# Optimization experiments

Measured on AMD Instinct MI355X. Metric: run time of the kernel, lower is better.

## Reference

```python
import jax, jax.numpy as jnp
import numpy as np

N = 100000      # num POIs (nodes)
M = 20000       # num trajectories (hyperedges)
NNZ = 1000000   # incidence entries
D = 128         # emb_dim
NUM_LAYERS = 3
NEG_SLOPE = 0.2  # PyG HypergraphConv leaky_relu default


def setup_inputs() -> dict:
    key = jax.random.key(0)
    ks = jax.random.split(key, 8)
    pois_embs = jax.random.normal(ks[0], (N, D), jnp.float32)
    traj_embs = jax.random.normal(ks[1], (M, D), jnp.float32)
    hyperedge_weight = jax.random.uniform(ks[2], (M,), jnp.float32)
    node_idx = jax.random.randint(ks[3], (NNZ,), 0, N, jnp.int32)
    edge_idx = jax.random.randint(ks[4], (NNZ,), 0, M, jnp.int32)
    # learned params of the shared HypergraphConv layer (heads=1, concat)
    W_lin = jax.random.normal(ks[5], (D, D), jnp.float32) / np.sqrt(D).astype(np.float32)
    att = jax.random.normal(ks[6], (2 * D,), jnp.float32) * 0.1
    bias = jnp.zeros((D,), jnp.float32)
    return dict(pois_embs=pois_embs, traj_embs=traj_embs,
                hyperedge_weight=hyperedge_weight,
                node_idx=node_idx, edge_idx=edge_idx,
                W_lin=W_lin, att=att, bias=bias)


def _segment_softmax(scores, seg, num_seg):
    smax = jax.ops.segment_max(scores, seg, num_segments=num_seg)
    smax = jnp.where(jnp.isfinite(smax), smax, 0.0)  # guard empty segments
    ex = jnp.exp(scores - smax[seg])
    den = jax.ops.segment_sum(ex, seg, num_segments=num_seg)
    return ex / (den[seg] + 1e-16)


def _hconv(x, traj_embs, hyperedge_weight, node_idx, edge_idx, W_lin, att, bias):
    # x: [N, D] node feats; traj_embs: [M, D] hyperedge feats
    xt = x @ W_lin            # [N, D]  lin(x)
    et = traj_embs @ W_lin    # [M, D]  lin(hyperedge_attr)
    # attention logits per incidence pair (additive decomposition of cat*att)
    s_n = xt @ att[:D]        # [N]
    s_e = et @ att[D:]        # [M]
    alpha = jax.nn.leaky_relu(s_n[node_idx] + s_e[edge_idx], NEG_SLOPE)  # [NNZ]
    alpha = _segment_softmax(alpha, node_idx, N)  # softmax grouped by node
    # degree normalizations: D = sum_e H_ve * w_e, B = |e|
    Ddeg = jax.ops.segment_sum(hyperedge_weight[edge_idx], node_idx, num_segments=N)
    Dinv = jnp.where(Ddeg > 0, 1.0 / Ddeg, 0.0)
    Bdeg = jax.ops.segment_sum(jnp.ones((NNZ,), xt.dtype), edge_idx, num_segments=M)
    Binv = jnp.where(Bdeg > 0, 1.0 / Bdeg, 0.0)
    # node -> edge: B^{-1} H^T (alpha * x)
    msg1 = (alpha * Binv[edge_idx])[:, None] * xt[node_idx]        # [NNZ, D]
    edge_out = jax.ops.segment_sum(msg1, edge_idx, num_segments=M)  # [M, D]
    # edge -> node: D^{-1} H (alpha * edge_out)
    msg2 = (alpha * Dinv[node_idx])[:, None] * edge_out[edge_idx]   # [NNZ, D]
    out = jax.ops.segment_sum(msg2, node_idx, num_segments=N)       # [N, D]
    return out + bias


def reference(pois_embs, traj_embs, hyperedge_weight, node_idx, edge_idx, W_lin, att, bias):
    cur = pois_embs
    acc = pois_embs  # running sum of stacked layer outputs (incl. input)
    for _ in range(NUM_LAYERS):
        cur = _hconv(cur, traj_embs, hyperedge_weight, node_idx, edge_idx, W_lin, att, bias) + cur
        acc = acc + cur
    return acc / jnp.asarray(NUM_LAYERS + 1, acc.dtype)  # mean over stack
```

## Files before the change

kernel.cpp:

```cpp
#include <hip/hip_runtime.h>
#include <hip/hip_fp16.h>
#include <cstdint>
#include <cstddef>
#include <cstring>

#define DIM 128
#define NEG_SLOPE 0.2f

#define EREP 16
#define NREP 8

typedef _Float16 half8v __attribute__((ext_vector_type(8)));
typedef __attribute__((ext_vector_type(4))) float float4v;

__device__ __forceinline__ float2 h2f2(uint u) {
  __half2 h;
  __builtin_memcpy(&h, &u, 4);
  return __half22float2(h);
}
__device__ __forceinline__ uint packh2(float lo, float hi) {
  __half2 h = __floats2half2_rn(lo, hi);
  uint u;
  __builtin_memcpy(&u, &h, 4);
  return u;
}
__device__ __forceinline__ ushort f2h_us(float f) {
  __half h = __float2half_rn(f);
  ushort us;
  __builtin_memcpy(&us, &h, 2);
  return us;
}
__device__ __forceinline__ float lrelu(float x) {
  return x >= 0.0f ? x : NEG_SLOPE * x;
}

__global__ void wswz_kernel(const float* __restrict__ W, ushort* __restrict__ Wswz)
{
  int i = blockIdx.x * 256 + threadIdx.x;
  int j = i & 7, lane = (i >> 3) & 63, nt = (i >> 9) & 7, kt = i >> 12;
  int k = kt * 32 + (lane >> 4) * 8 + j;
  int col = nt * 16 + (lane & 15);
  Wswz[i] = f2h_us(W[k * 128 + col]);
}

__global__ void poish_kernel(const float* __restrict__ pois,
                             uint4* __restrict__ pois_h, int N_, int NP)
{
  int i = blockIdx.x * 256 + threadIdx.x;
  if (i >= NP * 16) return;
  int row = i >> 4;
  uint4 o;
  if (row < N_) {
    const float* src = pois + (size_t)i * 8;
    float4 f0 = *(const float4*)src;
    float4 f1 = *(const float4*)(src + 4);
    o.x = packh2(f0.x, f0.y); o.y = packh2(f0.z, f0.w);
    o.z = packh2(f1.x, f1.y); o.w = packh2(f1.z, f1.w);
  } else { o.x = o.y = o.z = o.w = 0; }
  pois_h[i] = o;
}

__global__ __launch_bounds__(256) void gemm_mfma_kernel(
    const ushort* __restrict__ Xb, const ushort* __restrict__ Wswz,
    const float* __restrict__ att, ushort* __restrict__ Yb,
    float* __restrict__ s_n, int rowsN)
{
  __shared__ ushort st[64 * 128];
  int tid = threadIdx.x;
  int w = tid >> 6, lane = tid & 63;
  int q = lane >> 4, c = lane & 15;
  int r0b = blockIdx.x * 64;
  int r0 = r0b + w * 16;
  float4v acc[8];
#pragma unroll
  for (int nt = 0; nt < 8; ++nt) acc[nt] = (float4v){0.f, 0.f, 0.f, 0.f};
  const ushort* arow = Xb + (size_t)(r0 + c) * DIM + q * 8;
#pragma unroll
  for (int kt = 0; kt < 4; ++kt) {
    half8v a = *(const half8v*)(arow + kt * 32);
#pragma unroll
    for (int nt = 0; nt < 8; ++nt) {
      half8v b = *(const half8v*)(Wswz + ((((kt << 3) + nt) << 9) + (lane << 3)));
      acc[nt] = __builtin_amdgcn_mfma_f32_16x16x32_f16(a, b, acc[nt], 0, 0, 0);
    }
  }
  float av[8];
#pragma unroll
  for (int nt = 0; nt < 8; ++nt) av[nt] = att[nt * 16 + c];
  float p0 = 0, p1 = 0, p2 = 0, p3 = 0;
#pragma unroll
  for (int nt = 0; nt < 8; ++nt) {
    p0 = fmaf(acc[nt][0], av[nt], p0);
    p1 = fmaf(acc[nt][1], av[nt], p1);
    p2 = fmaf(acc[nt][2], av[nt], p2);
    p3 = fmaf(acc[nt][3], av[nt], p3);
  }
#pragma unroll
  for (int m = 8; m >= 1; m >>= 1) {
    p0 += __shfl_xor(p0, m, 64);
    p1 += __shfl_xor(p1, m, 64);
    p2 += __shfl_xor(p2, m, 64);
    p3 += __shfl_xor(p3, m, 64);
  }
  if (c == 0) {
    int rb = r0 + q * 4;
    if (rb + 0 < rowsN) s_n[rb + 0] = p0;
    if (rb + 1 < rowsN) s_n[rb + 1] = p1;
    if (rb + 2 < rowsN) s_n[rb + 2] = p2;
    if (rb + 3 < rowsN) s_n[rb + 3] = p3;
  }
  ushort* sw = st + w * 2048;
#pragma unroll
  for (int nt = 0; nt < 8; ++nt) {
    sw[(q * 4 + 0) * 128 + nt * 16 + c] = f2h_us(acc[nt][0]);
    sw[(q * 4 + 1) * 128 + nt * 16 + c] = f2h_us(acc[nt][1]);
    sw[(q * 4 + 2) * 128 + nt * 16 + c] = f2h_us(acc[nt][2]);
    sw[(q * 4 + 3) * 128 + nt * 16 + c] = f2h_us(acc[nt][3]);
  }
  __syncthreads();
#pragma unroll
  for (int it = 0; it < 4; ++it) {
    int idx = tid + it * 256;
    int row = idx >> 4, seg = idx & 15;
    *(uint4*)(Yb + (size_t)(r0b + row) * DIM + seg * 8) =
        *(const uint4*)&st[row * 128 + seg * 8];
  }
}

__global__ __launch_bounds__(256) void se_kernel(
    const float* __restrict__ traj, const float* __restrict__ W,
    const float* __restrict__ att, const float* __restrict__ hw,
    float* __restrict__ s_e, float2* __restrict__ se_hw, int M_)
{
  __shared__ float wv[128];
  int tid = threadIdx.x;
  if (tid < 128) {
    const float* wr = W + (size_t)tid * 128;
    float acc = 0.0f;
#pragma unroll 4
    for (int k = 0; k < 128; ++k) acc = fmaf(wr[k], att[DIM + k], acc);
    wv[tid] = acc;
  }
  __syncthreads();
  int e = blockIdx.x * 4 + (tid >> 6);
  int lane = tid & 63;
  if (e >= M_) return;
  const float* row = traj + (size_t)e * DIM;
  float v = row[lane] * wv[lane] + row[lane + 64] * wv[lane + 64];
#pragma unroll
  for (int d = 32; d > 0; d >>= 1) v += __shfl_down(v, d, 64);
  if (lane == 0) {
    s_e[e] = v;
    float2 g; g.x = v; g.y = hw[e];
    se_hw[e] = g;
  }
}

__global__ void hist_rank_kernel(const int* __restrict__ node_idx,
                                 const int* __restrict__ edge_idx,
                                 int* __restrict__ ncnt_r, int* __restrict__ ecnt_r,
                                 int* __restrict__ r_n, int* __restrict__ r_e,
                                 int nnz, int M_, int N_)
{
  int t = blockIdx.x * blockDim.x + threadIdx.x;
  int j = t * 2;
  if (j >= nnz) return;
  int* ec = ecnt_r + (size_t)(t & (EREP - 1)) * M_;
  int* nc = ncnt_r + (size_t)(t & (NREP - 1)) * N_;
  if (j + 2 <= nnz) {
    int2 e = *(const int2*)&edge_idx[j];
    int2 n = *(const int2*)&node_idx[j];
    int a0 = atomicAdd(&ec[e.x], 1);
    int a1 = atomicAdd(&ec[e.y], 1);
    int b0 = atomicAdd(&nc[n.x], 1);
    int b1 = atomicAdd(&nc[n.y], 1);
    *(int2*)&r_e[j] = make_int2(a0, a1);
    *(int2*)&r_n[j] = make_int2(b0, b1);
  } else {
    r_e[j] = atomicAdd(&ec[edge_idx[j]], 1);
    r_n[j] = atomicAdd(&nc[node_idx[j]], 1);
  }
}

__global__ void repsum_kernel(int* __restrict__ cnt_r, int* __restrict__ cnt,
                              int nbins, int reps)
{
  int b = blockIdx.x * blockDim.x + threadIdx.x;
  if (b >= nbins) return;
  int s = 0;
  for (int r = 0; r < reps; ++r) {
    size_t o = (size_t)r * nbins + b;
    int v = cnt_r[o];
    cnt_r[o] = s;
    s += v;
  }
  cnt[b] = s;
}

__global__ __launch_bounds__(1024) void scan_block_kernel(
    const int* __restrict__ cnt, int* __restrict__ off,
    int* __restrict__ partials, int nbins)
{
  __shared__ int ws[16];
  int tid = threadIdx.x, lane = tid & 63, wid = tid >> 6;
  int base = blockIdx.x * 4096 + tid * 4;
  int x0 = base + 0 < nbins ? cnt[base + 0] : 0;
  int x1 = base + 1 < nbins ? cnt[base + 1] : 0;
  int x2 = base + 2 < nbins ? cnt[base + 2] : 0;
  int x3 = base + 3 < nbins ? cnt[base + 3] : 0;
  int t = x0 + x1 + x2 + x3;
  int v = t;
#pragma unroll
  for (int d = 1; d < 64; d <<= 1) {
    int y = __shfl_up(v, d, 64);
    if (lane >= d) v += y;
  }
  if (lane == 63) ws[wid] = v;
  __syncthreads();
  if (tid < 16) {
    int s = ws[tid];
#pragma unroll
    for (int d = 1; d < 16; d <<= 1) {
      int y = __shfl_up(s, d, 16);
      if (tid >= d) s += y;
    }
    ws[tid] = s;
  }
  __syncthreads();
  int pre = (wid > 0 ? ws[wid - 1] : 0) + (v - t);
  if (base + 0 < nbins) off[base + 0] = pre;
  if (base + 1 < nbins) off[base + 1] = pre + x0;
  if (base + 2 < nbins) off[base + 2] = pre + x0 + x1;
  if (base + 3 < nbins) off[base + 3] = pre + x0 + x1 + x2;
  if (tid == 0) partials[blockIdx.x] = ws[15];
}

__global__ __launch_bounds__(64) void scan_partials_kernel(
    int* __restrict__ partials, int nb)
{
  int lane = threadIdx.x;
  int t = lane < nb ? partials[lane] : 0;
  int v = t;
#pragma unroll
  for (int d = 1; d < 64; d <<= 1) {
    int y = __shfl_up(v, d, 64);
    if (lane >= d) v += y;
  }
  if (lane < nb) partials[lane] = v - t;
  if (lane == 63) partials[nb] = v;
}

__global__ void add_off_combine_kernel(int* __restrict__ off,
                                       const int* __restrict__ partials,
                                       int* __restrict__ pre,
                                       int nbins, int nb, int reps)
{
  int i = blockIdx.x * blockDim.x + threadIdx.x;
  if (i < nbins) {
    int o = off[i] + partials[i >> 12];
    off[i] = o;
    for (int r = 0; r < reps; ++r) pre[(size_t)r * nbins + i] += o;
  }
  if (i == 0) off[nbins] = partials[nb];
}

__global__ void scatter_edge_kernel(const int* __restrict__ node_idx,
                                    const int* __restrict__ edge_idx,
                                    const int* __restrict__ r_e,
                                    const int* __restrict__ pre_e,
                                    int* __restrict__ nd_e, int nnz, int M_)
{
  int j = (blockIdx.x * blockDim.x + threadIdx.x) * 4;
  if (j >= nnz) return;
  if (j + 4 <= nnz) {
    const int* p0 = pre_e + (size_t)((j >> 1) & (EREP - 1)) * M_;
    const int* p1 = pre_e + (size_t)(((j >> 1) + 1) & (EREP - 1)) * M_;
    int4 e = *(const int4*)&edge_idx[j];
    int4 n = *(const int4*)&node_idx[j];
    int4 re = *(const int4*)&r_e[j];
    nd_e[p0[e.x] + re.x] = n.x;
    nd_e[p0[e.y] + re.y] = n.y;
    nd_e[p1[e.z] + re.z] = n.z;
    nd_e[p1[e.w] + re.w] = n.w;
  } else {
    for (int k = j; k < nnz; ++k) {
      const int* pp = pre_e + (size_t)((k >> 1) & (EREP - 1)) * M_;
      nd_e[pp[edge_idx[k]] + r_e[k]] = node_idx[k];
    }
  }
}

__global__ void scatter_node_kernel(const int* __restrict__ node_idx,
                                    const int* __restrict__ edge_idx,
                                    const int* __restrict__ r_n,
                                    const int* __restrict__ pre_n,
                                    int* __restrict__ eidx_n, int nnz, int N_)
{
  int j = (blockIdx.x * blockDim.x + threadIdx.x) * 4;
  if (j >= nnz) return;
  if (j + 4 <= nnz) {
    const int* p0 = pre_n + (size_t)((j >> 1) & (NREP - 1)) * N_;
    const int* p1 = pre_n + (size_t)(((j >> 1) + 1) & (NREP - 1)) * N_;
    int4 e = *(const int4*)&edge_idx[j];
    int4 n = *(const int4*)&node_idx[j];
    int4 rn = *(const int4*)&r_n[j];
    eidx_n[p0[n.x] + rn.x] = e.x;
    eidx_n[p0[n.y] + rn.y] = e.y;
    eidx_n[p1[n.z] + rn.z] = e.z;
    eidx_n[p1[n.w] + rn.w] = e.w;
  } else {
    for (int k = j; k < nnz; ++k) {
      const int* pp = pre_n + (size_t)((k >> 1) & (NREP - 1)) * N_;
      eidx_n[pp[node_idx[k]] + r_n[k]] = edge_idx[k];
    }
  }
}

__global__ void softstat_kernel(const int* __restrict__ noff,
                                const int* __restrict__ eidx_n,
                                const float* __restrict__ s_n,
                                const float2* __restrict__ se_hw,
                                float2* __restrict__ ns2,
                                float* __restrict__ Dinv, int N_)
{
  int n = blockIdx.x * blockDim.x + threadIdx.x;
  if (n >= N_) return;
  int s = noff[n], e1 = noff[n + 1];
  float sn = s_n[n];
  float m = -INFINITY, den = 0.0f, d = 0.0f;
  int t = s;
  for (; t + 4 <= e1; t += 4) {
    int i0 = eidx_n[t], i1 = eidx_n[t + 1], i2 = eidx_n[t + 2], i3 = eidx_n[t + 3];
    float2 g0 = se_hw[i0], g1 = se_hw[i1], g2 = se_hw[i2], g3 = se_hw[i3];
    float l0 = lrelu(sn + g0.x), l1 = lrelu(sn + g1.x);
    float l2 = lrelu(sn + g2.x), l3 = lrelu(sn + g3.x);
    float mm = fmaxf(fmaxf(fmaxf(l0, l1), fmaxf(l2, l3)), m);
    den = den * __expf(m - mm) + __expf(l0 - mm) + __expf(l1 - mm)
        + __expf(l2 - mm) + __expf(l3 - mm);
    m = mm;
    d += g0.y + g1.y + g2.y + g3.y;
  }
  for (; t < e1; ++t) {
    float2 g = se_hw[eidx_n[t]];
    float l = lrelu(sn + g.x);
    float mm = fmaxf(l, m);
    den = den * __expf(m - mm) + __expf(l - mm);
    m = mm;
    d += g.y;
  }
  if (s == e1) m = 0.0f;
  float2 r;
  r.x = sn;
  r.y = m + __logf(den + 1e-16f);
  ns2[n] = r;
  Dinv[n] = d > 0.0f ? 1.0f / d : 0.0f;
}

__global__ __launch_bounds__(256) void msg1_kernel(
    const int* __restrict__ eoff, const int* __restrict__ nd_e,
    const float2* __restrict__ ns2, const float* __restrict__ s_e,
    const ushort* __restrict__ xt, uint* __restrict__ eo, int M_)
{
  int e = blockIdx.x * (blockDim.x >> 6) + (threadIdx.x >> 6);
  int lane = threadIdx.x & 63;
  if (e >= M_) return;
  int s = eoff[e], t1 = eoff[e + 1];
  int len = t1 - s;
  float binv = len > 0 ? 1.0f / (float)len : 0.0f;
  float se = s_e[e];
  const uint* xt4 = (const uint*)xt + lane;
  float2 acc = {0.0f, 0.0f};
  int t = s;
  for (; t + 8 <= t1; t += 8) {
    int n0 = nd_e[t],     n1 = nd_e[t + 1], n2 = nd_e[t + 2], n3 = nd_e[t + 3];
    int n4 = nd_e[t + 4], n5 = nd_e[t + 5], n6 = nd_e[t + 6], n7 = nd_e[t + 7];
    float2 q0 = ns2[n0], q1 = ns2[n1], q2 = ns2[n2], q3 = ns2[n3];
    float2 q4 = ns2[n4], q5 = ns2[n5], q6 = ns2[n6], q7 = ns2[n7];
    uint u0 = xt4[(size_t)n0 * 64], u1 = xt4[(size_t)n1 * 64];
    uint u2 = xt4[(size_t)n2 * 64], u3 = xt4[(size_t)n3 * 64];
    uint u4 = xt4[(size_t)n4 * 64], u5 = xt4[(size_t)n5 * 64];
    uint u6 = xt4[(size_t)n6 * 64], u7 = xt4[(size_t)n7 * 64];
    float c0 = __expf(lrelu(q0.x + se) - q0.y);
    float c1 = __expf(lrelu(q1.x + se) - q1.y);
    float c2 = __expf(lrelu(q2.x + se) - q2.y);
    float c3 = __expf(lrelu(q3.x + se) - q3.y);
    float c4 = __expf(lrelu(q4.x + se) - q4.y);
    float c5 = __expf(lrelu(q5.x + se) - q5.y);
    float c6 = __expf(lrelu(q6.x + se) - q6.y);
    float c7 = __expf(lrelu(q7.x + se) - q7.y);
    float2 f0 = h2f2(u0), f1 = h2f2(u1), f2 = h2f2(u2), f3 = h2f2(u3);
    float2 f4 = h2f2(u4), f5 = h2f2(u5), f6 = h2f2(u6), f7 = h2f2(u7);
    acc.x = fmaf(c0, f0.x, acc.x); acc.y = fmaf(c0, f0.y, acc.y);
    acc.x = fmaf(c1, f1.x, acc.x); acc.y = fmaf(c1, f1.y, acc.y);
    acc.x = fmaf(c2, f2.x, acc.x); acc.y = fmaf(c2, f2.y, acc.y);
    acc.x = fmaf(c3, f3.x, acc.x); acc.y = fmaf(c3, f3.y, acc.y);
    acc.x = fmaf(c4, f4.x, acc.x); acc.y = fmaf(c4, f4.y, acc.y);
    acc.x = fmaf(c5, f5.x, acc.x); acc.y = fmaf(c5, f5.y, acc.y);
    acc.x = fmaf(c6, f6.x, acc.x); acc.y = fmaf(c6, f6.y, acc.y);
    acc.x = fmaf(c7, f7.x, acc.x); acc.y = fmaf(c7, f7.y, acc.y);
  }
  for (; t < t1; ++t) {
    int nd = nd_e[t];
    float2 q = ns2[nd];
    uint u = xt4[(size_t)nd * 64];
    float c = __expf(lrelu(q.x + se) - q.y);
    float2 f = h2f2(u);
    acc.x = fmaf(c, f.x, acc.x);
    acc.y = fmaf(c, f.y, acc.y);
  }
  eo[(size_t)e * (DIM / 2) + lane] = packh2(acc.x * binv, acc.y * binv);
}

__global__ __launch_bounds__(256) void msg2_kernel(
    const int* __restrict__ noff, const int* __restrict__ eidx_n,
    const float2* __restrict__ ns2, const float* __restrict__ Dinv,
    const float* __restrict__ s_e, const uint* __restrict__ eo,
    const float* __restrict__ bias,
    const float* __restrict__ cin_f, const uint* __restrict__ cin_h,
    const float* __restrict__ x1f, const uint* __restrict__ x2h,
    uint* __restrict__ couth, float* __restrict__ dout,
    int mode, int N_)
{
  int n = blockIdx.x * (blockDim.x >> 6) + (threadIdx.x >> 6);
  int lane = threadIdx.x & 63;
  if (n >= N_) return;
  int s = noff[n], t1 = noff[n + 1];
  float2 nsv = ns2[n];
  float sn = nsv.x, lz = nsv.y;
  const uint* eo4 = eo + lane;
  float2 acc = {0.0f, 0.0f};
  int t = s;
  for (; t + 8 <= t1; t += 8) {
    int e0 = eidx_n[t],     e1 = eidx_n[t + 1], e2 = eidx_n[t + 2], e3 = eidx_n[t + 3];
    int e4 = eidx_n[t + 4], e5 = eidx_n[t + 5], e6 = eidx_n[t + 6], e7 = eidx_n[t + 7];
    float x0 = s_e[e0], xx1 = s_e[e1], xx2 = s_e[e2], x3 = s_e[e3];
    float x4 = s_e[e4], x5 = s_e[e5], x6 = s_e[e6], x7 = s_e[e7];
    uint u0 = eo4[(size_t)e0 * 64], u1 = eo4[(size_t)e1 * 64];
    uint u2 = eo4[(size_t)e2 * 64], u3 = eo4[(size_t)e3 * 64];
    uint u4 = eo4[(size_t)e4 * 64], u5 = eo4[(size_t)e5 * 64];
    uint u6 = eo4[(size_t)e6 * 64], u7 = eo4[(size_t)e7 * 64];
    float c0 = __expf(lrelu(sn + x0) - lz);
    float c1 = __expf(lrelu(sn + xx1) - lz);
    float c2 = __expf(lrelu(sn + xx2) - lz);
    float c3 = __expf(lrelu(sn + x3) - lz);
    float c4 = __expf(lrelu(sn + x4) - lz);
    float c5 = __expf(lrelu(sn + x5) - lz);
    float c6 = __expf(lrelu(sn + x6) - lz);
    float c7 = __expf(lrelu(sn + x7) - lz);
    float2 f0 = h2f2(u0), f1 = h2f2(u1), f2 = h2f2(u2), f3 = h2f2(u3);
    float2 f4 = h2f2(u4), f5 = h2f2(u5), f6 = h2f2(u6), f7 = h2f2(u7);
    acc.x = fmaf(c0, f0.x, acc.x); acc.y = fmaf(c0, f0.y, acc.y);
    acc.x = fmaf(c1, f1.x, acc.x); acc.y = fmaf(c1, f1.y, acc.y);
    acc.x = fmaf(c2, f2.x, acc.x); acc.y = fmaf(c2, f2.y, acc.y);
    acc.x = fmaf(c3, f3.x, acc.x); acc.y = fmaf(c3, f3.y, acc.y);
    acc.x = fmaf(c4, f4.x, acc.x); acc.y = fmaf(c4, f4.y, acc.y);
    acc.x = fmaf(c5, f5.x, acc.x); acc.y = fmaf(c5, f5.y, acc.y);
    acc.x = fmaf(c6, f6.x, acc.x); acc.y = fmaf(c6, f6.y, acc.y);
    acc.x = fmaf(c7, f7.x, acc.x); acc.y = fmaf(c7, f7.y, acc.y);
  }
  for (; t < t1; ++t) {
    int e = eidx_n[t];
    uint u = eo4[(size_t)e * 64];
    float c = __expf(lrelu(sn + s_e[e]) - lz);
    float2 f = h2f2(u);
    acc.x = fmaf(c, f.x, acc.x);
    acc.y = fmaf(c, f.y, acc.y);
  }
  float sc = Dinv[n];
  float2 b = ((const float2*)bias)[lane];
  size_t idx = (size_t)n * DIM + lane * 2;
  float cinx, ciny;
  if (mode == 0) {
    cinx = cin_f[idx]; ciny = cin_f[idx + 1];
  } else {
    float2 f = h2f2(cin_h[(size_t)n * 64 + lane]);
    cinx = f.x; ciny = f.y;
  }
  float cx = cinx + acc.x * sc + b.x;
  float cy = ciny + acc.y * sc + b.y;
  if (mode == 2) {
    float2 f2v = h2f2(x2h[(size_t)n * 64 + lane]);
    dout[idx]     = (x1f[idx]     + f2v.x + cinx + cx) * 0.25f;
    dout[idx + 1] = (x1f[idx + 1] + f2v.y + ciny + cy) * 0.25f;
  } else {
    couth[(size_t)n * 64 + lane] = packh2(cx, cy);
  }
}

static inline int cdiv(int a, int b) { return (a + b - 1) / b; }

extern "C" void kernel_launch(void* const* d_in, const int* in_sizes, int n_in,
                              void* d_out, int out_size, void* d_ws, size_t ws_size,
                              hipStream_t stream)
{
  const float* pois = (const float*)d_in[0];
  const float* traj = (const float*)d_in[1];
  const float* hw   = (const float*)d_in[2];
  const int* node_idx = (const int*)d_in[3];
  const int* edge_idx = (const int*)d_in[4];
  const float* W    = (const float*)d_in[5];
  const float* att  = (const float*)d_in[6];
  const float* bias = (const float*)d_in[7];
  float* dout = (float*)d_out;

  const int N   = in_sizes[0] / DIM;
  const int M   = in_sizes[2];
  const int NNZ = in_sizes[3];
  const int NP  = (N + 63) & ~63;

  char* p = (char*)d_ws;
  auto alloc = [&](size_t bytes) -> void* {
    void* r = (void*)p;
    p += (bytes + 255) & ~(size_t)255;
    return r;
  };
  ushort* xt_h    = (ushort*)alloc((size_t)NP * DIM * 2);
  ushort* pois_h  = (ushort*)alloc((size_t)NP * DIM * 2);
  uint*   cura_h  = (uint*)alloc((size_t)NP * 64 * 4);
  uint*   curb_h  = (uint*)alloc((size_t)NP * 64 * 4);
  ushort* W_swz   = (ushort*)alloc(16384 * 2);
  uint*   eo_h  = (uint*)alloc((size_t)M * (DIM / 2) * 4);
  float2* ns2   = (float2*)alloc((size_t)N * 8);
  float*  s_e  = (float*)alloc((size_t)M * 4);
  float2* se_hw = (float2*)alloc((size_t)M * 8);
  float*  s_n  = (float*)alloc((size_t)N * 4);
  float*  Dinv = (float*)alloc((size_t)N * 4);
  int* ecnt   = (int*)alloc((size_t)M * 4);
  int* ncnt   = (int*)alloc((size_t)N * 4);
  int* ecnt_r = (int*)alloc((size_t)EREP * M * 4);
  int* ncnt_r = (int*)alloc((size_t)NREP * N * 4);
  int* eoff = (int*)alloc((size_t)(M + 1) * 4);
  int* noff = (int*)alloc((size_t)(N + 1) * 4);
  int* r_e  = (int*)alloc((size_t)NNZ * 4);
  int* r_n  = (int*)alloc((size_t)NNZ * 4);
  int* nd_e   = (int*)alloc((size_t)NNZ * 4);
  int* eidx_n = (int*)alloc((size_t)NNZ * 4);
  int* part_e = (int*)alloc(65 * 4);
  int* part_n = (int*)alloc(65 * 4);
  (void)ws_size;

  const int nbE = cdiv(M, 4096), nbN = cdiv(N, 4096);

  hipMemsetAsync(ecnt_r, 0, (size_t)EREP * M * 4, stream);
  hipMemsetAsync(ncnt_r, 0, (size_t)NREP * N * 4, stream);
  hist_rank_kernel<<<cdiv(NNZ, 512), 256, 0, stream>>>(node_idx, edge_idx, ncnt_r, ecnt_r, r_n, r_e, NNZ, M, N);
  repsum_kernel<<<cdiv(M, 256), 256, 0, stream>>>(ecnt_r, ecnt, M, EREP);
  repsum_kernel<<<cdiv(N, 256), 256, 0, stream>>>(ncnt_r, ncnt, N, NREP);
  scan_block_kernel<<<nbE, 1024, 0, stream>>>(ecnt, eoff, part_e, M);
  scan_block_kernel<<<nbN, 1024, 0, stream>>>(ncnt, noff, part_n, N);
  scan_partials_kernel<<<1, 64, 0, stream>>>(part_e, nbE);
  scan_partials_kernel<<<1, 64, 0, stream>>>(part_n, nbN);
  add_off_combine_kernel<<<cdiv(M, 256), 256, 0, stream>>>(eoff, part_e, ecnt_r, M, nbE, EREP);
  add_off_combine_kernel<<<cdiv(N, 256), 256, 0, stream>>>(noff, part_n, ncnt_r, N, nbN, NREP);
  scatter_edge_kernel<<<cdiv(NNZ, 1024), 256, 0, stream>>>(node_idx, edge_idx, r_e, ecnt_r, nd_e, NNZ, M);
  scatter_node_kernel<<<cdiv(NNZ, 1024), 256, 0, stream>>>(node_idx, edge_idx, r_n, ncnt_r, eidx_n, NNZ, N);

  wswz_kernel<<<64, 256, 0, stream>>>(W, W_swz);
  se_kernel<<<cdiv(M, 4), 256, 0, stream>>>(traj, W, att, hw, s_e, se_hw, M);
  poish_kernel<<<cdiv(NP * 16, 256), 256, 0, stream>>>(pois, (uint4*)pois_h, N, NP);

  for (int layer = 0; layer < 3; ++layer) {
    const ushort* gin = (layer == 0) ? pois_h
                       : (layer == 1) ? (const ushort*)cura_h
                                      : (const ushort*)curb_h;
    gemm_mfma_kernel<<<NP / 64, 256, 0, stream>>>(gin, W_swz, att, xt_h, s_n, N);
    softstat_kernel<<<cdiv(N, 256), 256, 0, stream>>>(noff, eidx_n, s_n, se_hw, ns2, Dinv, N);
    msg1_kernel<<<cdiv(M, 4), 256, 0, stream>>>(eoff, nd_e, ns2, s_e, xt_h, eo_h, M);
    const uint* cin_h = (layer == 1) ? cura_h : curb_h;
    uint* couth = (layer == 0) ? cura_h : curb_h;
    msg2_kernel<<<cdiv(N, 4), 256, 0, stream>>>(noff, eidx_n, ns2, Dinv, s_e, eo_h,
                                                bias, pois, cin_h, pois, cura_h,
                                                couth, dout, layer, N);
  }
}
```

Measured before the change: 738.5 us.

## Split each wave into four row-groups with 16-byte gathers in message kernels

```diff
diff --git a/kernel.cpp b/kernel.cpp
--- a/kernel.cpp
+++ b/kernel.cpp
@@ -359,131 +359,153 @@
 __global__ __launch_bounds__(256) void msg1_kernel(
     const int* __restrict__ eoff, const int* __restrict__ nd_e,
     const float2* __restrict__ ns2, const float* __restrict__ s_e,
-    const ushort* __restrict__ xt, uint* __restrict__ eo, int M_)
-{
-  int e = blockIdx.x * (blockDim.x >> 6) + (threadIdx.x >> 6);
+    const uint4* __restrict__ xt16, uint4* __restrict__ eo16, int M_)
+{
+  int e = blockIdx.x * 4 + (threadIdx.x >> 6);
   int lane = threadIdx.x & 63;
+  int r = lane >> 4, c = lane & 15;
   if (e >= M_) return;
   int s = eoff[e], t1 = eoff[e + 1];
   int len = t1 - s;
   float binv = len > 0 ? 1.0f / (float)len : 0.0f;
   float se = s_e[e];
-  const uint* xt4 = (const uint*)xt + lane;
-  float2 acc = {0.0f, 0.0f};
-  int t = s;
-  for (; t + 8 <= t1; t += 8) {
-    int n0 = nd_e[t],     n1 = nd_e[t + 1], n2 = nd_e[t + 2], n3 = nd_e[t + 3];
-    int n4 = nd_e[t + 4], n5 = nd_e[t + 5], n6 = nd_e[t + 6], n7 = nd_e[t + 7];
-    float2 q0 = ns2[n0], q1 = ns2[n1], q2 = ns2[n2], q3 = ns2[n3];
-    float2 q4 = ns2[n4], q5 = ns2[n5], q6 = ns2[n6], q7 = ns2[n7];
-    uint u0 = xt4[(size_t)n0 * 64], u1 = xt4[(size_t)n1 * 64];
-    uint u2 = xt4[(size_t)n2 * 64], u3 = xt4[(size_t)n3 * 64];
-    uint u4 = xt4[(size_t)n4 * 64], u5 = xt4[(size_t)n5 * 64];
-    uint u6 = xt4[(size_t)n6 * 64], u7 = xt4[(size_t)n7 * 64];
-    float c0 = __expf(lrelu(q0.x + se) - q0.y);
-    float c1 = __expf(lrelu(q1.x + se) - q1.y);
-    float c2 = __expf(lrelu(q2.x + se) - q2.y);
-    float c3 = __expf(lrelu(q3.x + se) - q3.y);
-    float c4 = __expf(lrelu(q4.x + se) - q4.y);
-    float c5 = __expf(lrelu(q5.x + se) - q5.y);
-    float c6 = __expf(lrelu(q6.x + se) - q6.y);
-    float c7 = __expf(lrelu(q7.x + se) - q7.y);
-    float2 f0 = h2f2(u0), f1 = h2f2(u1), f2 = h2f2(u2), f3 = h2f2(u3);
-    float2 f4 = h2f2(u4), f5 = h2f2(u5), f6 = h2f2(u6), f7 = h2f2(u7);
-    acc.x = fmaf(c0, f0.x, acc.x); acc.y = fmaf(c0, f0.y, acc.y);
-    acc.x = fmaf(c1, f1.x, acc.x); acc.y = fmaf(c1, f1.y, acc.y);
-    acc.x = fmaf(c2, f2.x, acc.x); acc.y = fmaf(c2, f2.y, acc.y);
-    acc.x = fmaf(c3, f3.x, acc.x); acc.y = fmaf(c3, f3.y, acc.y);
-    acc.x = fmaf(c4, f4.x, acc.x); acc.y = fmaf(c4, f4.y, acc.y);
-    acc.x = fmaf(c5, f5.x, acc.x); acc.y = fmaf(c5, f5.y, acc.y);
-    acc.x = fmaf(c6, f6.x, acc.x); acc.y = fmaf(c6, f6.y, acc.y);
-    acc.x = fmaf(c7, f7.x, acc.x); acc.y = fmaf(c7, f7.y, acc.y);
-  }
-  for (; t < t1; ++t) {
-    int nd = nd_e[t];
-    float2 q = ns2[nd];
-    uint u = xt4[(size_t)nd * 64];
-    float c = __expf(lrelu(q.x + se) - q.y);
-    float2 f = h2f2(u);
-    acc.x = fmaf(c, f.x, acc.x);
-    acc.y = fmaf(c, f.y, acc.y);
-  }
-  eo[(size_t)e * (DIM / 2) + lane] = packh2(acc.x * binv, acc.y * binv);
+  float acc[8];
+#pragma unroll
+  for (int j = 0; j < 8; ++j) acc[j] = 0.0f;
+  for (int t = s; t < t1; t += 8) {
+#pragma unroll
+    for (int h = 0; h < 2; ++h) {
+      int tb = t + h * 4;
+      if (tb < t1) {
+        int ti = tb + r;
+        int tc = ti < t1 ? ti : t1 - 1;
+        float valid = ti < t1 ? 1.0f : 0.0f;
+        int nd = nd_e[tc];
+        float2 q = ns2[nd];
+        float coef = valid * __expf(lrelu(q.x + se) - q.y);
+        uint4 g = xt16[(size_t)nd * 16 + c];
+        float2 f0 = h2f2(g.x), f1 = h2f2(g.y), f2 = h2f2(g.z), f3 = h2f2(g.w);
+        acc[0] = fmaf(coef, f0.x, acc[0]);
+        acc[1] = fmaf(coef, f0.y, acc[1]);
+        acc[2] = fmaf(coef, f1.x, acc[2]);
+        acc[3] = fmaf(coef, f1.y, acc[3]);
+        acc[4] = fmaf(coef, f2.x, acc[4]);
+        acc[5] = fmaf(coef, f2.y, acc[5]);
+        acc[6] = fmaf(coef, f3.x, acc[6]);
+        acc[7] = fmaf(coef, f3.y, acc[7]);
+      }
+    }
+  }
+#pragma unroll
+  for (int j = 0; j < 8; ++j) {
+    acc[j] += __shfl_xor(acc[j], 16, 64);
+    acc[j] += __shfl_xor(acc[j], 32, 64);
+  }
+  if (r == 0) {
+    uint4 o;
+    o.x = packh2(acc[0] * binv, acc[1] * binv);
+    o.y = packh2(acc[2] * binv, acc[3] * binv);
+    o.z = packh2(acc[4] * binv, acc[5] * binv);
+    o.w = packh2(acc[6] * binv, acc[7] * binv);
+    eo16[(size_t)e * 16 + c] = o;
+  }
 }
 
 __global__ __launch_bounds__(256) void msg2_kernel(
     const int* __restrict__ noff, const int* __restrict__ eidx_n,
     const float2* __restrict__ ns2, const float* __restrict__ Dinv,
-    const float* __restrict__ s_e, const uint* __restrict__ eo,
+    const float* __restrict__ s_e, const uint4* __restrict__ eo16,
     const float* __restrict__ bias,
-    const float* __restrict__ cin_f, const uint* __restrict__ cin_h,
-    const float* __restrict__ x1f, const uint* __restrict__ x2h,
-    uint* __restrict__ couth, float* __restrict__ dout,
+    const float* __restrict__ cin_f, const uint4* __restrict__ cin_h16,
+    const float* __restrict__ x1f, const uint4* __restrict__ x2h16,
+    uint4* __restrict__ couth16, float* __restrict__ dout,
     int mode, int N_)
 {
-  int n = blockIdx.x * (blockDim.x >> 6) + (threadIdx.x >> 6);
+  int n = blockIdx.x * 4 + (threadIdx.x >> 6);
   int lane = threadIdx.x & 63;
+  int r = lane >> 4, c = lane & 15;
   if (n >= N_) return;
   int s = noff[n], t1 = noff[n + 1];
   float2 nsv = ns2[n];
   float sn = nsv.x, lz = nsv.y;
-  const uint* eo4 = eo + lane;
-  float2 acc = {0.0f, 0.0f};
-  int t = s;
-  for (; t + 8 <= t1; t += 8) {
-    int e0 = eidx_n[t],     e1 = eidx_n[t + 1], e2 = eidx_n[t + 2], e3 = eidx_n[t + 3];
-    int e4 = eidx_n[t + 4], e5 = eidx_n[t + 5], e6 = eidx_n[t + 6], e7 = eidx_n[t + 7];
-    float x0 = s_e[e0], xx1 = s_e[e1], xx2 = s_e[e2], x3 = s_e[e3];
-    float x4 = s_e[e4], x5 = s_e[e5], x6 = s_e[e6], x7 = s_e[e7];
-    uint u0 = eo4[(size_t)e0 * 64], u1 = eo4[(size_t)e1 * 64];
-    uint u2 = eo4[(size_t)e2 * 64], u3 = eo4[(size_t)e3 * 64];
-    uint u4 = eo4[(size_t)e4 * 64], u5 = eo4[(size_t)e5 * 64];
-    uint u6 = eo4[(size_t)e6 * 64], u7 = eo4[(size_t)e7 * 64];
-    float c0 = __expf(lrelu(sn + x0) - lz);
-    float c1 = __expf(lrelu(sn + xx1) - lz);
-    float c2 = __expf(lrelu(sn + xx2) - lz);
-    float c3 = __expf(lrelu(sn + x3) - lz);
-    float c4 = __expf(lrelu(sn + x4) - lz);
-    float c5 = __expf(lrelu(sn + x5) - lz);
-    float c6 = __expf(lrelu(sn + x6) - lz);
-    float c7 = __expf(lrelu(sn + x7) - lz);
-    float2 f0 = h2f2(u0), f1 = h2f2(u1), f2 = h2f2(u2), f3 = h2f2(u3);
-    float2 f4 = h2f2(u4), f5 = h2f2(u5), f6 = h2f2(u6), f7 = h2f2(u7);
-    acc.x = fmaf(c0, f0.x, acc.x); acc.y = fmaf(c0, f0.y, acc.y);
-    acc.x = fmaf(c1, f1.x, acc.x); acc.y = fmaf(c1, f1.y, acc.y);
-    acc.x = fmaf(c2, f2.x, acc.x); acc.y = fmaf(c2, f2.y, acc.y);
-    acc.x = fmaf(c3, f3.x, acc.x); acc.y = fmaf(c3, f3.y, acc.y);
-    acc.x = fmaf(c4, f4.x, acc.x); acc.y = fmaf(c4, f4.y, acc.y);
-    acc.x = fmaf(c5, f5.x, acc.x); acc.y = fmaf(c5, f5.y, acc.y);
-    acc.x = fmaf(c6, f6.x, acc.x); acc.y = fmaf(c6, f6.y, acc.y);
-    acc.x = fmaf(c7, f7.x, acc.x); acc.y = fmaf(c7, f7.y, acc.y);
-  }
-  for (; t < t1; ++t) {
-    int e = eidx_n[t];
-    uint u = eo4[(size_t)e * 64];
-    float c = __expf(lrelu(sn + s_e[e]) - lz);
-    float2 f = h2f2(u);
-    acc.x = fmaf(c, f.x, acc.x);
-    acc.y = fmaf(c, f.y, acc.y);
-  }
+  float acc[8];
+#pragma unroll
+  for (int j = 0; j < 8; ++j) acc[j] = 0.0f;
+  for (int t = s; t < t1; t += 8) {
+#pragma unroll
+    for (int h = 0; h < 2; ++h) {
+      int tb = t + h * 4;
+      if (tb < t1) {
+        int ti = tb + r;
+        int tc = ti < t1 ? ti : t1 - 1;
+        float valid = ti < t1 ? 1.0f : 0.0f;
+        int ed = eidx_n[tc];
+        float xs = s_e[ed];
+        float coef = valid * __expf(lrelu(sn + xs) - lz);
+        uint4 g = eo16[(size_t)ed * 16 + c];
+        float2 f0 = h2f2(g.x), f1 = h2f2(g.y), f2 = h2f2(g.z), f3 = h2f2(g.w);
+        acc[0] = fmaf(coef, f0.x, acc[0]);
+        acc[1] = fmaf(coef, f0.y, acc[1]);
+        acc[2] = fmaf(coef, f1.x, acc[2]);
+        acc[3] = fmaf(coef, f1.y, acc[3]);
+        acc[4] = fmaf(coef, f2.x, acc[4]);
+        acc[5] = fmaf(coef, f2.y, acc[5]);
+        acc[6] = fmaf(coef, f3.x, acc[6]);
+        acc[7] = fmaf(coef, f3.y, acc[7]);
+      }
+    }
+  }
+#pragma unroll
+  for (int j = 0; j < 8; ++j) {
+    acc[j] += __shfl_xor(acc[j], 16, 64);
+    acc[j] += __shfl_xor(acc[j], 32, 64);
+  }
+  if (r != 0) return;
   float sc = Dinv[n];
-  float2 b = ((const float2*)bias)[lane];
-  size_t idx = (size_t)n * DIM + lane * 2;
-  float cinx, ciny;
+  float cin[8];
   if (mode == 0) {
-    cinx = cin_f[idx]; ciny = cin_f[idx + 1];
+    const float4* cf = (const float4*)(cin_f + (size_t)n * DIM);
+    float4 a = cf[c * 2], b = cf[c * 2 + 1];
+    cin[0] = a.x; cin[1] = a.y; cin[2] = a.z; cin[3] = a.w;
+    cin[4] = b.x; cin[5] = b.y; cin[6] = b.z; cin[7] = b.w;
   } else {
-    float2 f = h2f2(cin_h[(size_t)n * 64 + lane]);
-    cinx = f.x; ciny = f.y;
-  }
-  float cx = cinx + acc.x * sc + b.x;
-  float cy = ciny + acc.y * sc + b.y;
+    uint4 ch = cin_h16[(size_t)n * 16 + c];
+    float2 p0 = h2f2(ch.x), p1 = h2f2(ch.y), p2 = h2f2(ch.z), p3 = h2f2(ch.w);
+    cin[0] = p0.x; cin[1] = p0.y; cin[2] = p1.x; cin[3] = p1.y;
+    cin[4] = p2.x; cin[5] = p2.y; cin[6] = p3.x; cin[7] = p3.y;
+  }
+  const float4* bf = (const float4*)bias;
+  float4 ba = bf[c * 2], bb = bf[c * 2 + 1];
+  float bs[8] = {ba.x, ba.y, ba.z, ba.w, bb.x, bb.y, bb.z, bb.w};
+  float cx[8];
+#pragma unroll
+  for (int j = 0; j < 8; ++j) cx[j] = cin[j] + acc[j] * sc + bs[j];
   if (mode == 2) {
-    float2 f2v = h2f2(x2h[(size_t)n * 64 + lane]);
-    dout[idx]     = (x1f[idx]     + f2v.x + cinx + cx) * 0.25f;
-    dout[idx + 1] = (x1f[idx + 1] + f2v.y + ciny + cy) * 0.25f;
+    const float4* x1 = (const float4*)(x1f + (size_t)n * DIM);
+    float4 xa = x1[c * 2], xb = x1[c * 2 + 1];
+    float x1v[8] = {xa.x, xa.y, xa.z, xa.w, xb.x, xb.y, xb.z, xb.w};
+    uint4 x2 = x2h16[(size_t)n * 16 + c];
+    float2 y0 = h2f2(x2.x), y1 = h2f2(x2.y), y2 = h2f2(x2.z), y3 = h2f2(x2.w);
+    float x2v[8] = {y0.x, y0.y, y1.x, y1.y, y2.x, y2.y, y3.x, y3.y};
+    float4 o0, o1;
+    o0.x = (x1v[0] + x2v[0] + cin[0] + cx[0]) * 0.25f;
+    o0.y = (x1v[1] + x2v[1] + cin[1] + cx[1]) * 0.25f;
+    o0.z = (x1v[2] + x2v[2] + cin[2] + cx[2]) * 0.25f;
+    o0.w = (x1v[3] + x2v[3] + cin[3] + cx[3]) * 0.25f;
+    o1.x = (x1v[4] + x2v[4] + cin[4] + cx[4]) * 0.25f;
+    o1.y = (x1v[5] + x2v[5] + cin[5] + cx[5]) * 0.25f;
+    o1.z = (x1v[6] + x2v[6] + cin[6] + cx[6]) * 0.25f;
+    o1.w = (x1v[7] + x2v[7] + cin[7] + cx[7]) * 0.25f;
+    float4* dp = (float4*)(dout + (size_t)n * DIM);
+    dp[c * 2] = o0;
+    dp[c * 2 + 1] = o1;
   } else {
-    couth[(size_t)n * 64 + lane] = packh2(cx, cy);
+    uint4 o;
+    o.x = packh2(cx[0], cx[1]);
+    o.y = packh2(cx[2], cx[3]);
+    o.z = packh2(cx[4], cx[5]);
+    o.w = packh2(cx[6], cx[7]);
+    couth16[(size_t)n * 16 + c] = o;
   }
 }
 
@@ -565,11 +587,14 @@
                                       : (const ushort*)curb_h;
     gemm_mfma_kernel<<<NP / 64, 256, 0, stream>>>(gin, W_swz, att, xt_h, s_n, N);
     softstat_kernel<<<cdiv(N, 256), 256, 0, stream>>>(noff, eidx_n, s_n, se_hw, ns2, Dinv, N);
-    msg1_kernel<<<cdiv(M, 4), 256, 0, stream>>>(eoff, nd_e, ns2, s_e, xt_h, eo_h, M);
+    msg1_kernel<<<cdiv(M, 4), 256, 0, stream>>>(eoff, nd_e, ns2, s_e,
+                                                (const uint4*)xt_h, (uint4*)eo_h, M);
     const uint* cin_h = (layer == 1) ? cura_h : curb_h;
     uint* couth = (layer == 0) ? cura_h : curb_h;
-    msg2_kernel<<<cdiv(N, 4), 256, 0, stream>>>(noff, eidx_n, ns2, Dinv, s_e, eo_h,
-                                                bias, pois, cin_h, pois, cura_h,
-                                                couth, dout, layer, N);
-  }
-}
+    msg2_kernel<<<cdiv(N, 4), 256, 0, stream>>>(noff, eidx_n, ns2, Dinv, s_e,
+                                                (const uint4*)eo_h, bias,
+                                                pois, (const uint4*)cin_h,
+                                                pois, (const uint4*)cura_h,
+                                                (uint4*)couth, dout, layer, N);
+  }
+}
```

After: 691.4 us. 6.4% less time.
